# Optimization experiments

Hardware: AMD Instinct MI355X
Metric: run time of the kernel (lower is better)

Reference implementation:

```python
import jax, jax.numpy as jnp
import numpy as np

B, N, M, C_IN, C_OUT = 8, 1024, 1024, 8, 16
C_REP = C_IN + 1  # density channel + in_channels


def setup_inputs() -> dict:
    key = jax.random.key(0)
    ks = jax.random.split(key, 6)
    x = jax.random.normal(ks[0], (B, N, 1), dtype=jnp.float32)
    y = jax.random.normal(ks[1], (B, N, C_IN), dtype=jnp.float32)
    t = jax.random.normal(ks[2], (B, M, 1), dtype=jnp.float32)
    # sigma initialised as log(init_length_scale) * ones(in_channels+1)
    sigma = jnp.full((C_REP,), np.log(0.1), dtype=jnp.float32)
    W = jax.random.normal(ks[3], (C_OUT, C_REP), dtype=jnp.float32) / np.sqrt(C_REP)
    b = jnp.zeros((C_OUT,), dtype=jnp.float32)
    return {"x": x, "y": y, "t": t, "sigma": sigma, "W": W, "b": b}


def reference(x, y, t, sigma, W, b):
    # pairwise squared distances: (B, N, M)
    dists = (x - jnp.swapaxes(t, 1, 2)) ** 2
    # RBF weights with per-channel length scales: (B, N, M, C_REP)
    scales = jnp.exp(sigma)  # (C_REP,)
    wt = jnp.exp(-0.5 * dists[..., None] / scales**2)
    # prepend density channel of ones to y: (B, N, C_REP)
    y_rep = jnp.concatenate([jnp.ones_like(y[..., :1]), y], axis=-1)
    # weighted sum over context points n -> (B, M, C_REP)
    y_out = jnp.sum(y_rep[:, :, None, :] * wt, axis=1)
    density, conv = y_out[..., :1], y_out[..., 1:]
    y_out = jnp.concatenate([density, conv / (density + 1e-8)], axis=-1)
    # pointwise linear: (B, M, C_OUT)
    return jnp.einsum("bmc,oc->bmo", y_out, W) + b
```

## Files before the change

### kernel.cpp

```cpp
#include <hip/hip_runtime.h>


#define B_     8
#define N_     1024
#define M_     1024
#define CIN    8
#define COUT   16
#define CREP   9
#define NSPLIT 2
#define NCHUNK (N_ / NSPLIT)
#define LM     8
#define GN     32
#define RM     2
#define MTILE  (LM * RM)
#define KITER  (NCHUNK / GN)

#if __has_builtin(__builtin_amdgcn_exp2f)
#define EXP2F(v) __builtin_amdgcn_exp2f(v)
#else
#define EXP2F(v) exp2f(v)
#endif

__global__ __launch_bounds__(256) void convcnp_partial(
    const float* __restrict__ x,
    const float* __restrict__ y,
    const float* __restrict__ t,
    const float* __restrict__ sigma,
    float* __restrict__ P)
{
    __shared__ float x_lds[NCHUNK];
    __shared__ float y_lds[NCHUNK * CIN];
    __shared__ float red[4][LM][RM][CREP];

    const int tid  = threadIdx.x;
    const int tile = blockIdx.x & 63;
    const int s    = (blockIdx.x >> 6) & (NSPLIT - 1);
    const int bb   = blockIdx.x >> 7;
    const int m0   = tile * MTILE;
    const int n0   = s * NCHUNK;

    const float4* x4  = (const float4*)(x + bb * N_ + n0);
    float4*       xl4 = (float4*)x_lds;
    if (tid < NCHUNK / 4) xl4[tid] = x4[tid];
    const float4* y4  = (const float4*)(y + (bb * N_ + n0) * CIN);
    float4*       yl4 = (float4*)y_lds;
#pragma unroll
    for (int j = 0; j < NCHUNK * CIN / 4 / 256; ++j)
        yl4[tid + j * 256] = y4[tid + j * 256];

    float kc[CREP];
#pragma unroll
    for (int c = 0; c < CREP; ++c)
        kc[c] = -0.72134752044f * EXP2F(-2.88539008178f * sigma[c]);
    bool uni = true;
#pragma unroll
    for (int c = 1; c < CREP; ++c) uni = uni && (kc[c] == kc[0]);

    const int   ml = tid & (LM - 1);
    const int   g  = tid >> 3;
    const float t0 = t[bb * M_ + m0 + ml];
    const float t1 = t[bb * M_ + m0 + ml + LM];

    float acc[RM][CREP];
#pragma unroll
    for (int r = 0; r < RM; ++r)
#pragma unroll
        for (int c = 0; c < CREP; ++c) acc[r][c] = 0.f;

    __syncthreads();

    if (uni) {
        const float k0 = kc[0];
#pragma unroll 4
        for (int k = 0; k < KITER; ++k) {
            const int    n  = g + (k << 5);
            const float  xv = x_lds[n];
            const float4 ya = *(const float4*)(y_lds + n * CIN);
            const float4 yb = *(const float4*)(y_lds + n * CIN + 4);
            float d0 = xv - t0; d0 *= d0;
            float d1 = xv - t1; d1 *= d1;
            const float w0 = EXP2F(k0 * d0);
            const float w1 = EXP2F(k0 * d1);
            acc[0][0] += w0;
            acc[0][1] += ya.x * w0; acc[0][2] += ya.y * w0;
            acc[0][3] += ya.z * w0; acc[0][4] += ya.w * w0;
            acc[0][5] += yb.x * w0; acc[0][6] += yb.y * w0;
            acc[0][7] += yb.z * w0; acc[0][8] += yb.w * w0;
            acc[1][0] += w1;
            acc[1][1] += ya.x * w1; acc[1][2] += ya.y * w1;
            acc[1][3] += ya.z * w1; acc[1][4] += ya.w * w1;
            acc[1][5] += yb.x * w1; acc[1][6] += yb.y * w1;
            acc[1][7] += yb.z * w1; acc[1][8] += yb.w * w1;
        }
    } else {
#pragma unroll 2
        for (int k = 0; k < KITER; ++k) {
            const int    n  = g + (k << 5);
            const float  xv = x_lds[n];
            const float4 ya = *(const float4*)(y_lds + n * CIN);
            const float4 yb = *(const float4*)(y_lds + n * CIN + 4);
            float d0 = xv - t0; d0 *= d0;
            float d1 = xv - t1; d1 *= d1;
            const float yr[CREP] = {1.f, ya.x, ya.y, ya.z, ya.w,
                                         yb.x, yb.y, yb.z, yb.w};
#pragma unroll
            for (int c = 0; c < CREP; ++c) {
                acc[0][c] += yr[c] * EXP2F(kc[c] * d0);
                acc[1][c] += yr[c] * EXP2F(kc[c] * d1);
            }
        }
    }

    const int wave = tid >> 6;
    const int lane = tid & 63;
#pragma unroll
    for (int r = 0; r < RM; ++r)
#pragma unroll
        for (int c = 0; c < CREP; ++c) {
            float v = acc[r][c];
            v += __shfl_xor(v, 8, 64);
            v += __shfl_xor(v, 16, 64);
            v += __shfl_xor(v, 32, 64);
            if (lane < LM) red[wave][lane][r][c] = v;
        }
    __syncthreads();

    if (tid < MTILE * CREP) {
        const int mm = tid / CREP;
        const int c  = tid - mm * CREP;
        const int r  = mm >> 3, l = mm & 7;
        const float v = red[0][l][r][c] + red[1][l][r][c] +
                        red[2][l][r][c] + red[3][l][r][c];
        P[((s * B_ + bb) * M_ + m0 + mm) * CREP + c] = v;
    }
}

__global__ __launch_bounds__(256) void convcnp_proj(
    const float* __restrict__ P,
    const float* __restrict__ W,
    const float* __restrict__ bias,
    float* __restrict__ out)
{
    const int gid = blockIdx.x * 256 + threadIdx.x;
    const int o   = gid & (COUT - 1);
    const int bm  = gid >> 4;
    const float* p0 = P + bm * CREP;
    const float* p1 = P + (size_t)B_ * M_ * CREP + bm * CREP;
    float p[CREP];
#pragma unroll
    for (int c = 0; c < CREP; ++c) p[c] = p0[c] + p1[c];
    const float dens = p[0];
    const float inv  = 1.0f / (dens + 1e-8f);
    float r = bias[o] + W[o * CREP] * dens;
#pragma unroll
    for (int c = 1; c < CREP; ++c) r += W[o * CREP + c] * (p[c] * inv);
    out[gid] = r;
}

extern "C" void kernel_launch(void* const* d_in, const int* in_sizes, int n_in,
                              void* d_out, int out_size, void* d_ws, size_t ws_size,
                              hipStream_t stream) {
    const float* x     = (const float*)d_in[0];
    const float* y     = (const float*)d_in[1];
    const float* t     = (const float*)d_in[2];
    const float* sigma = (const float*)d_in[3];
    const float* W     = (const float*)d_in[4];
    const float* bias  = (const float*)d_in[5];
    float*       out   = (float*)d_out;
    float*       P     = (float*)d_ws;

    convcnp_partial<<<dim3(B_ * (M_ / MTILE) * NSPLIT), dim3(256), 0, stream>>>(
        x, y, t, sigma, P);
    convcnp_proj<<<dim3(B_ * M_ * COUT / 256), dim3(256), 0, stream>>>(
        P, W, bias, out);
}
```

Before: 71.35 us.

## Fuse partial RBF accumulation and projection into one kernel without N split

Drops the two-way split over context points and computes the full N reduction per block, then applies the density normalisation and the pointwise linear projection in the same kernel through shared memory. This removes the second kernel launch and the workspace round trip for partial sums. In exchange the grid is halved to 512 blocks, each doing twice the loop work, and LDS use per block doubles to about 37KB. That can reduce occupancy and parallelism on a GPU with many CUs.

```diff
diff --git a/kernel.cpp b/kernel.cpp
--- a/kernel.cpp
+++ b/kernel.cpp
@@ -1,19 +1,17 @@
 #include <hip/hip_runtime.h>
 
 
-#define B_     8
-#define N_     1024
-#define M_     1024
-#define CIN    8
-#define COUT   16
-#define CREP   9
-#define NSPLIT 2
-#define NCHUNK (N_ / NSPLIT)
-#define LM     8
-#define GN     32
-#define RM     2
-#define MTILE  (LM * RM)
-#define KITER  (NCHUNK / GN)
+#define B_    8
+#define N_    1024
+#define M_    1024
+#define CIN   8
+#define COUT  16
+#define CREP  9
+#define LM    8
+#define GN    32
+#define RM    2
+#define MTILE (LM * RM)
+#define KITER (N_ / GN)
 
 #if __has_builtin(__builtin_amdgcn_exp2f)
 #define EXP2F(v) __builtin_amdgcn_exp2f(v)
@@ -21,32 +19,32 @@
 #define EXP2F(v) exp2f(v)
 #endif
 
-__global__ __launch_bounds__(256) void convcnp_partial(
+__global__ __launch_bounds__(256) void convcnp_fused(
     const float* __restrict__ x,
     const float* __restrict__ y,
     const float* __restrict__ t,
     const float* __restrict__ sigma,
-    float* __restrict__ P)
+    const float* __restrict__ W,
+    const float* __restrict__ bias,
+    float* __restrict__ out)
 {
-    __shared__ float x_lds[NCHUNK];
-    __shared__ float y_lds[NCHUNK * CIN];
+    __shared__ float x_lds[N_];
+    __shared__ float y_lds[N_ * CIN];
     __shared__ float red[4][LM][RM][CREP];
+    __shared__ float fin[MTILE][CREP];
 
     const int tid  = threadIdx.x;
+    const int bb   = blockIdx.x >> 6;
     const int tile = blockIdx.x & 63;
-    const int s    = (blockIdx.x >> 6) & (NSPLIT - 1);
-    const int bb   = blockIdx.x >> 7;
     const int m0   = tile * MTILE;
-    const int n0   = s * NCHUNK;
 
-    const float4* x4  = (const float4*)(x + bb * N_ + n0);
+    const float4* x4  = (const float4*)(x + bb * N_);
     float4*       xl4 = (float4*)x_lds;
-    if (tid < NCHUNK / 4) xl4[tid] = x4[tid];
-    const float4* y4  = (const float4*)(y + (bb * N_ + n0) * CIN);
+    xl4[tid] = x4[tid];
+    const float4* y4  = (const float4*)(y + bb * N_ * CIN);
     float4*       yl4 = (float4*)y_lds;
 #pragma unroll
-    for (int j = 0; j < NCHUNK * CIN / 4 / 256; ++j)
-        yl4[tid + j * 256] = y4[tid + j * 256];
+    for (int j = 0; j < 8; ++j) yl4[tid + j * 256] = y4[tid + j * 256];
 
     float kc[CREP];
 #pragma unroll
@@ -129,32 +127,19 @@
         const int mm = tid / CREP;
         const int c  = tid - mm * CREP;
         const int r  = mm >> 3, l = mm & 7;
-        const float v = red[0][l][r][c] + red[1][l][r][c] +
-                        red[2][l][r][c] + red[3][l][r][c];
-        P[((s * B_ + bb) * M_ + m0 + mm) * CREP + c] = v;
+        fin[mm][c] = red[0][l][r][c] + red[1][l][r][c] +
+                     red[2][l][r][c] + red[3][l][r][c];
     }
-}
+    __syncthreads();
 
-__global__ __launch_bounds__(256) void convcnp_proj(
-    const float* __restrict__ P,
-    const float* __restrict__ W,
-    const float* __restrict__ bias,
-    float* __restrict__ out)
-{
-    const int gid = blockIdx.x * 256 + threadIdx.x;
-    const int o   = gid & (COUT - 1);
-    const int bm  = gid >> 4;
-    const float* p0 = P + bm * CREP;
-    const float* p1 = P + (size_t)B_ * M_ * CREP + bm * CREP;
-    float p[CREP];
-#pragma unroll
-    for (int c = 0; c < CREP; ++c) p[c] = p0[c] + p1[c];
-    const float dens = p[0];
+    const int o = tid & 15;
+    const int m = tid >> 4;
+    const float dens = fin[m][0];
     const float inv  = 1.0f / (dens + 1e-8f);
     float r = bias[o] + W[o * CREP] * dens;
 #pragma unroll
-    for (int c = 1; c < CREP; ++c) r += W[o * CREP + c] * (p[c] * inv);
-    out[gid] = r;
+    for (int c = 1; c < CREP; ++c) r += W[o * CREP + c] * (fin[m][c] * inv);
+    out[(bb * M_ + m0 + m) * COUT + o] = r;
 }
 
 extern "C" void kernel_launch(void* const* d_in, const int* in_sizes, int n_in,
@@ -167,10 +152,7 @@
     const float* W     = (const float*)d_in[4];
     const float* bias  = (const float*)d_in[5];
     float*       out   = (float*)d_out;
-    float*       P     = (float*)d_ws;
 
-    convcnp_partial<<<dim3(B_ * (M_ / MTILE) * NSPLIT), dim3(256), 0, stream>>>(
-        x, y, t, sigma, P);
-    convcnp_proj<<<dim3(B_ * M_ * COUT / 256), dim3(256), 0, stream>>>(
-        P, W, bias, out);
+    convcnp_fused<<<dim3(B_ * (M_ / MTILE)), dim3(256), 0, stream>>>(
+        x, y, t, sigma, W, bias, out);
 }
```

After: 69.56 us. -2.5%, faster.
